# Optimization experiments

Measured on AMD Instinct MI355X. Metric: run time of the kernel, lower is better.

Reference implementation:

```python
import jax, jax.numpy as jnp
import numpy as np

NUM_FEATURES = 128
NUM_RADIAL = 6
NUM_ATOM_TYPES = 95
N_ATOMS = 100000
N_EDGES = 1000000


def setup_inputs() -> dict:
    key = jax.random.key(0)
    ks = jax.random.split(key, 8)
    Z = jax.random.randint(ks[0], (N_ATOMS,), 0, NUM_ATOM_TYPES, dtype=jnp.int32)
    rbf = jax.random.normal(ks[1], (N_EDGES, NUM_RADIAL), dtype=jnp.float32)
    idnb_i = jax.random.randint(ks[2], (N_EDGES,), 0, N_ATOMS, dtype=jnp.int32)
    idnb_j = jax.random.randint(ks[3], (N_EDGES,), 0, N_ATOMS, dtype=jnp.int32)
    # parameters
    s3 = np.sqrt(3.0).astype(np.float32)
    embeddings = jax.random.uniform(ks[4], (NUM_ATOM_TYPES, NUM_FEATURES), jnp.float32, -s3, s3)
    W_rbf = jax.random.normal(ks[5], (NUM_RADIAL, NUM_FEATURES), dtype=jnp.float32) * 0.3
    b_rbf = jnp.zeros((NUM_FEATURES,), jnp.float32)
    W = jax.random.normal(ks[6], (2 * NUM_FEATURES + NUM_RADIAL * 0 + 2 * NUM_FEATURES // (2 * NUM_FEATURES) * 0 + 2 * NUM_FEATURES + NUM_FEATURES - 2 * NUM_FEATURES, NUM_FEATURES), dtype=jnp.float32)  # placeholder, replaced below
    W = jax.random.normal(ks[6], (2 * NUM_FEATURES + NUM_FEATURES, NUM_FEATURES), dtype=jnp.float32) * 0.05  # (3F, F)
    b = jnp.zeros((NUM_FEATURES,), jnp.float32)
    return {"Z": Z, "rbf": rbf, "idnb_i": idnb_i, "idnb_j": idnb_j,
            "embeddings": embeddings, "W_rbf": W_rbf, "b_rbf": b_rbf, "W": W, "b": b}


def reference(Z, rbf, idnb_i, idnb_j, embeddings, W_rbf, b_rbf, W, b):
    act = jax.nn.swish
    # dense_rbf: [E, num_radial] -> [E, F]
    rbf_h = act(rbf @ W_rbf + b_rbf)
    # gather atom embeddings by atomic number, then by edge endpoints
    x = embeddings[Z]            # [N_atoms, F]
    x1 = x[idnb_i]               # [E, F]
    x2 = x[idnb_j]               # [E, F]
    h = jnp.concatenate([x1, x2, rbf_h], axis=-1)  # [E, 3F]
    return act(h @ W + b)        # [E, F]
```

## Files before the change

kernel.cpp:

```cpp
#include <hip/hip_runtime.h>
#include <hip/hip_bf16.h>
#include <stdint.h>

#define F 128
#define R 6
#define NTYPES 95
#define MTILE 128
#define HPAD 136

typedef short bf16x8 __attribute__((ext_vector_type(8)));
typedef float floatx4 __attribute__((ext_vector_type(4)));

__device__ __forceinline__ unsigned short f2bf(float x) {
    union { float f; unsigned u; } cv; cv.f = x;
    unsigned u = cv.u;
    return (unsigned short)((u + 0x7FFFu + ((u >> 16) & 1u)) >> 16);
}

__device__ __forceinline__ float swishf(float x) {
    return x / (1.0f + __expf(-x));
}

__global__ void prep_kernel(const float* __restrict__ emb,
                            const float* __restrict__ W,
                            float* __restrict__ embW,
                            unsigned short* __restrict__ w2t) {
    int t = threadIdx.x;
    int b = blockIdx.x;
    if (b < NTYPES) {
        int c = t >> 7, f = t & 127;
        const float* er = emb + b * F;
        const float* Wc = W + c * F * F;
        float a = 0.f;
        #pragma unroll 8
        for (int k = 0; k < F; ++k) a = __builtin_fmaf(er[k], Wc[k * F + f], a);
        embW[b * 256 + c * F + f] = a;
    } else {
        int idx = (b - NTYPES) * 256 + t;
        int n = idx >> 7, k = idx & 127;
        w2t[n * F + k] = f2bf(W[(256 + k) * F + n]);
    }
}

__global__ __launch_bounds__(256) void
edge_kernel(const int* __restrict__ Z,
            const float* __restrict__ rbf,
            const int* __restrict__ idnb_i,
            const int* __restrict__ idnb_j,
            const float* __restrict__ W_rbf,
            const float* __restrict__ b_rbf,
            const float* __restrict__ bvec,
            const float* __restrict__ embW,
            const unsigned short* __restrict__ w2t,
            float* __restrict__ out,
            int E) {
    __shared__ __align__(16) short h_bf[MTILE * HPAD];
    __shared__ float rbf_s[MTILE * R];
    __shared__ int zi_s[MTILE];
    __shared__ int zj_s[MTILE];
    __shared__ float bs[F];

    int t = threadIdx.x;
    int blk = blockIdx.x;
    long ebase = (long)blk * MTILE;

    #pragma unroll
    for (int i = 0; i < 3; ++i) {
        int idx = i * 256 + t;
        long g = ebase * R + idx;
        rbf_s[idx] = (g < (long)E * R) ? rbf[g] : 0.f;
    }
    if (t < MTILE) {
        long e = ebase + t;
        long ec = (e < (long)E) ? e : 0;
        zi_s[t] = Z[idnb_i[ec]];
        zj_s[t] = Z[idnb_j[ec]];
    }
    if (t < F) bs[t] = bvec[t];

    int fpair = t & 63;
    int f0 = fpair * 2;
    float wr0[R], wr1[R];
    #pragma unroll
    for (int r = 0; r < R; ++r) {
        wr0[r] = W_rbf[r * F + f0];
        wr1[r] = W_rbf[r * F + f0 + 1];
    }
    float brb0 = b_rbf[f0], brb1 = b_rbf[f0 + 1];

    __syncthreads();

    int eg = t >> 6;
    for (int it = 0; it < 32; ++it) {
        int e = eg * 32 + it;
        const float* rp = rbf_s + e * R;
        float v0 = brb0, v1 = brb1;
        #pragma unroll
        for (int r = 0; r < R; ++r) {
            float rv = rp[r];
            v0 = __builtin_fmaf(rv, wr0[r], v0);
            v1 = __builtin_fmaf(rv, wr1[r], v1);
        }
        v0 = swishf(v0); v1 = swishf(v1);
        unsigned packed = (unsigned)f2bf(v0) | ((unsigned)f2bf(v1) << 16);
        *(unsigned*)(&h_bf[e * HPAD + f0]) = packed;
    }

    __syncthreads();

    int w = t >> 6;
    int lid = t & 63;
    int quad = lid >> 4;
    int l15 = lid & 15;
    int wbase = w * 32;

    floatx4 acc[2][8];
    #pragma unroll
    for (int rt = 0; rt < 2; ++rt)
        #pragma unroll
        for (int c = 0; c < 8; ++c)
            acc[rt][c] = (floatx4){0.f, 0.f, 0.f, 0.f};

    const bf16x8* w2v = (const bf16x8*)w2t;
    #pragma unroll
    for (int ks = 0; ks < 4; ++ks) {
        bf16x8 a0 = *(const bf16x8*)(&h_bf[(wbase + l15) * HPAD + ks * 32 + quad * 8]);
        bf16x8 a1 = *(const bf16x8*)(&h_bf[(wbase + 16 + l15) * HPAD + ks * 32 + quad * 8]);
        #pragma unroll
        for (int c = 0; c < 8; ++c) {
            bf16x8 bfr = w2v[(c * 16 + l15) * 16 + ks * 4 + quad];
            acc[0][c] = __builtin_amdgcn_mfma_f32_16x16x32_bf16(a0, bfr, acc[0][c], 0, 0, 0);
            acc[1][c] = __builtin_amdgcn_mfma_f32_16x16x32_bf16(a1, bfr, acc[1][c], 0, 0, 0);
        }
    }

    #pragma unroll
    for (int rt = 0; rt < 2; ++rt) {
        #pragma unroll
        for (int rg = 0; rg < 4; ++rg) {
            int e_loc = wbase + rt * 16 + quad * 4 + rg;
            long e_g = ebase + e_loc;
            bool ok = e_g < (long)E;
            int zi = zi_s[e_loc], zj = zj_s[e_loc];
            const float* p0 = embW + zi * 256;
            const float* p1 = embW + zj * 256 + F;
            float* op = out + e_g * F;
            #pragma unroll
            for (int c = 0; c < 8; ++c) {
                int f = c * 16 + l15;
                float v = acc[rt][c][rg] + p0[f] + p1[f] + bs[f];
                v = swishf(v);
                if (ok) op[f] = v;
            }
        }
    }
}

extern "C" void kernel_launch(void* const* d_in, const int* in_sizes, int n_in,
                              void* d_out, int out_size, void* d_ws, size_t ws_size,
                              hipStream_t stream) {
    const int*   Z     = (const int*)d_in[0];
    const float* rbf   = (const float*)d_in[1];
    const int*   id_i  = (const int*)d_in[2];
    const int*   id_j  = (const int*)d_in[3];
    const float* emb   = (const float*)d_in[4];
    const float* W_rbf = (const float*)d_in[5];
    const float* b_rbf = (const float*)d_in[6];
    const float* W     = (const float*)d_in[7];
    const float* bvec  = (const float*)d_in[8];
    float* out = (float*)d_out;
    int E = in_sizes[2];

    float* embW = (float*)d_ws;
    unsigned short* w2t = (unsigned short*)((char*)d_ws + 97280);

    prep_kernel<<<NTYPES + 64, 256, 0, stream>>>(emb, W, embW, w2t);
    int grid = (E + MTILE - 1) / MTILE;
    edge_kernel<<<grid, 256, 0, stream>>>(Z, rbf, id_i, id_j, W_rbf, b_rbf, bvec,
                                          embW, w2t, out, E);
}
```

Before: 710.4 us.

## Transpose MFMA operands for vectorized float4 output stores and fold bias into embW

The MFMA operands are swapped so the weight fragment is the A operand and the edge tile is B. Each lane's accumulator then holds 4 consecutive features of one edge, which allows 128-bit embW loads and 128-bit output stores in place of scalar strided ones. The bias is folded into the precomputed embW table, the Z gather is spread across all 256 threads, rbf is read from LDS as float2, and the swish divide becomes a hardware reciprocal. The output write of the 512MB result is the main cost these changes target; the fast reciprocal slightly changes rounding.

```diff
diff --git a/kernel.cpp b/kernel.cpp
--- a/kernel.cpp
+++ b/kernel.cpp
@@ -18,11 +18,19 @@
 }
 
 __device__ __forceinline__ float swishf(float x) {
-    return x / (1.0f + __expf(-x));
+    return x * __builtin_amdgcn_rcpf(1.0f + __expf(-x));
+}
+
+__device__ __forceinline__ floatx4 swish4(floatx4 v) {
+    floatx4 r;
+    #pragma unroll
+    for (int i = 0; i < 4; ++i) r[i] = swishf(v[i]);
+    return r;
 }
 
 __global__ void prep_kernel(const float* __restrict__ emb,
                             const float* __restrict__ W,
+                            const float* __restrict__ bvec,
                             float* __restrict__ embW,
                             unsigned short* __restrict__ w2t) {
     int t = threadIdx.x;
@@ -34,7 +42,7 @@
         float a = 0.f;
         #pragma unroll 8
         for (int k = 0; k < F; ++k) a = __builtin_fmaf(er[k], Wc[k * F + f], a);
-        embW[b * 256 + c * F + f] = a;
+        embW[b * 256 + c * F + f] = a + (c == 0 ? bvec[f] : 0.f);
     } else {
         int idx = (b - NTYPES) * 256 + t;
         int n = idx >> 7, k = idx & 127;
@@ -49,7 +57,6 @@
             const int* __restrict__ idnb_j,
             const float* __restrict__ W_rbf,
             const float* __restrict__ b_rbf,
-            const float* __restrict__ bvec,
             const float* __restrict__ embW,
             const unsigned short* __restrict__ w2t,
             float* __restrict__ out,
@@ -58,7 +65,6 @@
     __shared__ float rbf_s[MTILE * R];
     __shared__ int zi_s[MTILE];
     __shared__ int zj_s[MTILE];
-    __shared__ float bs[F];
 
     int t = threadIdx.x;
     int blk = blockIdx.x;
@@ -70,13 +76,13 @@
         long g = ebase * R + idx;
         rbf_s[idx] = (g < (long)E * R) ? rbf[g] : 0.f;
     }
-    if (t < MTILE) {
-        long e = ebase + t;
+    {
+        int te = t & 127;
+        long e = ebase + te;
         long ec = (e < (long)E) ? e : 0;
-        zi_s[t] = Z[idnb_i[ec]];
-        zj_s[t] = Z[idnb_j[ec]];
+        int zz = Z[(t < 128 ? idnb_i : idnb_j)[ec]];
+        if (t < 128) zi_s[te] = zz; else zj_s[te] = zz;
     }
-    if (t < F) bs[t] = bvec[t];
 
     int fpair = t & 63;
     int f0 = fpair * 2;
@@ -93,13 +99,14 @@
     int eg = t >> 6;
     for (int it = 0; it < 32; ++it) {
         int e = eg * 32 + it;
-        const float* rp = rbf_s + e * R;
+        const float2* rp2 = (const float2*)(rbf_s + e * R);
+        float2 qa = rp2[0], qb = rp2[1], qc = rp2[2];
+        float rv[R] = {qa.x, qa.y, qb.x, qb.y, qc.x, qc.y};
         float v0 = brb0, v1 = brb1;
         #pragma unroll
         for (int r = 0; r < R; ++r) {
-            float rv = rp[r];
-            v0 = __builtin_fmaf(rv, wr0[r], v0);
-            v1 = __builtin_fmaf(rv, wr1[r], v1);
+            v0 = __builtin_fmaf(rv[r], wr0[r], v0);
+            v1 = __builtin_fmaf(rv[r], wr1[r], v1);
         }
         v0 = swishf(v0); v1 = swishf(v1);
         unsigned packed = (unsigned)f2bf(v0) | ((unsigned)f2bf(v1) << 16);
@@ -116,42 +123,39 @@
 
     floatx4 acc[2][8];
     #pragma unroll
-    for (int rt = 0; rt < 2; ++rt)
+    for (int et = 0; et < 2; ++et)
         #pragma unroll
-        for (int c = 0; c < 8; ++c)
-            acc[rt][c] = (floatx4){0.f, 0.f, 0.f, 0.f};
+        for (int ft = 0; ft < 8; ++ft)
+            acc[et][ft] = (floatx4){0.f, 0.f, 0.f, 0.f};
 
     const bf16x8* w2v = (const bf16x8*)w2t;
     #pragma unroll
     for (int ks = 0; ks < 4; ++ks) {
-        bf16x8 a0 = *(const bf16x8*)(&h_bf[(wbase + l15) * HPAD + ks * 32 + quad * 8]);
-        bf16x8 a1 = *(const bf16x8*)(&h_bf[(wbase + 16 + l15) * HPAD + ks * 32 + quad * 8]);
+        bf16x8 b0 = *(const bf16x8*)(&h_bf[(wbase + l15) * HPAD + ks * 32 + quad * 8]);
+        bf16x8 b1 = *(const bf16x8*)(&h_bf[(wbase + 16 + l15) * HPAD + ks * 32 + quad * 8]);
         #pragma unroll
-        for (int c = 0; c < 8; ++c) {
-            bf16x8 bfr = w2v[(c * 16 + l15) * 16 + ks * 4 + quad];
-            acc[0][c] = __builtin_amdgcn_mfma_f32_16x16x32_bf16(a0, bfr, acc[0][c], 0, 0, 0);
-            acc[1][c] = __builtin_amdgcn_mfma_f32_16x16x32_bf16(a1, bfr, acc[1][c], 0, 0, 0);
+        for (int ft = 0; ft < 8; ++ft) {
+            bf16x8 afr = w2v[(ft * 16 + l15) * 16 + ks * 4 + quad];
+            acc[0][ft] = __builtin_amdgcn_mfma_f32_16x16x32_bf16(afr, b0, acc[0][ft], 0, 0, 0);
+            acc[1][ft] = __builtin_amdgcn_mfma_f32_16x16x32_bf16(afr, b1, acc[1][ft], 0, 0, 0);
         }
     }
 
     #pragma unroll
-    for (int rt = 0; rt < 2; ++rt) {
+    for (int et = 0; et < 2; ++et) {
+        int e_loc = wbase + et * 16 + l15;
+        long e_g = ebase + e_loc;
+        bool ok = e_g < (long)E;
+        int zi = zi_s[e_loc], zj = zj_s[e_loc];
+        const floatx4* p0 = (const floatx4*)(embW + zi * 256);
+        const floatx4* p1 = (const floatx4*)(embW + zj * 256 + F);
+        float* op = out + e_g * F;
         #pragma unroll
-        for (int rg = 0; rg < 4; ++rg) {
-            int e_loc = wbase + rt * 16 + quad * 4 + rg;
-            long e_g = ebase + e_loc;
-            bool ok = e_g < (long)E;
-            int zi = zi_s[e_loc], zj = zj_s[e_loc];
-            const float* p0 = embW + zi * 256;
-            const float* p1 = embW + zj * 256 + F;
-            float* op = out + e_g * F;
-            #pragma unroll
-            for (int c = 0; c < 8; ++c) {
-                int f = c * 16 + l15;
-                float v = acc[rt][c][rg] + p0[f] + p1[f] + bs[f];
-                v = swishf(v);
-                if (ok) op[f] = v;
-            }
+        for (int ft = 0; ft < 8; ++ft) {
+            int f4 = ft * 4 + quad;
+            floatx4 v = acc[et][ft] + p0[f4] + p1[f4];
+            floatx4 r = swish4(v);
+            if (ok) *(floatx4*)(op + f4 * 4) = r;
         }
     }
 }
@@ -174,8 +178,8 @@
     float* embW = (float*)d_ws;
     unsigned short* w2t = (unsigned short*)((char*)d_ws + 97280);
 
-    prep_kernel<<<NTYPES + 64, 256, 0, stream>>>(emb, W, embW, w2t);
+    prep_kernel<<<NTYPES + 64, 256, 0, stream>>>(emb, W, bvec, embW, w2t);
     int grid = (E + MTILE - 1) / MTILE;
-    edge_kernel<<<grid, 256, 0, stream>>>(Z, rbf, id_i, id_j, W_rbf, b_rbf, bvec,
+    edge_kernel<<<grid, 256, 0, stream>>>(Z, rbf, id_i, id_j, W_rbf, b_rbf,
                                           embW, w2t, out, E);
 }
```

Measured after the change: 768.4 us. 1.08x slower.
